# Performance work log

Measured on AMD Instinct MI355X. Metric: run time of the kernel, lower is better.

The kernel has to match this reference:

```python
import jax, jax.numpy as jnp
import numpy as np

IN_F, OUT_F = 512, 512
GRID_SIZE, SPLINE_ORDER = 5, 3
K = GRID_SIZE + SPLINE_ORDER  # 8 basis functions
B, S = 8, 1024


def setup_inputs() -> dict:
    key = jax.random.key(0)
    k1, k2, k3, k4, k5 = jax.random.split(key, 5)
    return {
        "x": jax.random.normal(k1, (B, S, IN_F), dtype=jnp.float32),
        "coeff": jax.random.normal(k2, (OUT_F, IN_F, K), dtype=jnp.float32),
        "scale_base": jax.random.normal(k3, (OUT_F, IN_F), dtype=jnp.float32) * 0.1,
        "scale_spline": jax.random.normal(k4, (OUT_F, IN_F), dtype=jnp.float32),
        "base_bias": jax.random.normal(k5, (OUT_F, IN_F), dtype=jnp.float32),
    }


def reference(x, coeff, scale_base, scale_spline, base_bias):
    batch = x.shape[0]
    in_f = x.shape[-1]
    k = coeff.shape[-1]

    xc = jnp.clip(x.reshape(-1, in_f), -1.0, 1.0)      # (N, in)
    base = jax.nn.silu(xc)                              # (N, in)

    # polynomial basis recurrence: b0 = 1, b1 = x, b_i = 2*x*b_{i-1} - 1
    bases = [jnp.ones_like(xc), xc]
    for _ in range(2, k):
        bases.append(2.0 * xc * bases[-1] - 1.0)
    basis = jnp.stack(bases[:k], axis=-1)               # (N, in, K)

    # spline[n,o] = sum_{i,k} scale_spline[o,i]*coeff[o,i,k]*basis[n,i,k]
    w_spline = scale_spline[..., None] * coeff          # (out, in, K)
    spline_term = jnp.einsum('nik,oik->no', basis, w_spline)
    base_term = base @ scale_base.T                     # (N, out)
    out = base_term + spline_term + jnp.sum(base_bias, axis=1)  # (N, out)

    out = out.reshape(batch, -1, base_bias.shape[0])    # (B, S, out)
    if out.shape[-2] == 1:
        out = out[..., 0, :]
    return out
```

## Files before the change

kernel.cpp:

```cpp
#include <hip/hip_runtime.h>
#include <hip/hip_bf16.h>

#define IN_FEAT 512
#define OUT_FEAT 512
#define NTOK 8192
#define KDIM 4096

#define BM 64
#define BN 128
#define BK 64

typedef short bf16x8 __attribute__((ext_vector_type(8)));
typedef float f32x4 __attribute__((ext_vector_type(4)));

static __device__ inline short f2bf(float f) {
    union { float f; unsigned u; } v; v.f = f;
    unsigned u = v.u;
    u += 0x7fffu + ((u >> 16) & 1u);
    return (short)(u >> 16);
}

static __device__ inline unsigned pack2bf(float f0, float f1) {
    union { float f; unsigned u; } a, b; a.f = f0; b.f = f1;
    return __builtin_amdgcn_perm(b.u + 0x8000u, a.u + 0x8000u, 0x07060302u);
}

static __device__ inline void gload_lds16(const short* g, short* l) {
    __builtin_amdgcn_global_load_lds(
        (const __attribute__((address_space(1))) unsigned int*)g,
        (__attribute__((address_space(3))) unsigned int*)l,
        16, 0, 0);
}

__global__ __launch_bounds__(256) void kan_prep(
    const float* __restrict__ coeff, const float* __restrict__ scale_base,
    const float* __restrict__ scale_spline, const float* __restrict__ base_bias,
    short* __restrict__ Wb, float* __restrict__ bias)
{
    int o = blockIdx.x;
    int tid = threadIdx.x;
    float local = 0.f;
#pragma unroll
    for (int rep = 0; rep < 2; ++rep) {
        int i = tid + rep * 256;
        size_t oi = (size_t)o * IN_FEAT + i;
        const float4* c4 = (const float4*)(coeff + oi * 8);
        float4 ca = c4[0], cb = c4[1];
        float ss = scale_spline[oi];
        float sb = scale_base[oi];
        local += base_bias[oi] + ss * ca.x;
        bf16x8 w;
        w[0] = f2bf(sb);
        w[1] = f2bf(ss * ca.y); w[2] = f2bf(ss * ca.z); w[3] = f2bf(ss * ca.w);
        w[4] = f2bf(ss * cb.x); w[5] = f2bf(ss * cb.y); w[6] = f2bf(ss * cb.z);
        w[7] = f2bf(ss * cb.w);
        *(bf16x8*)(Wb + (size_t)o * KDIM + (size_t)i * 8) = w;
    }
    __shared__ float red[4];
    for (int off = 32; off > 0; off >>= 1) local += __shfl_down(local, off, 64);
    int lane = tid & 63, wv = tid >> 6;
    if (lane == 0) red[wv] = local;
    __syncthreads();
    if (tid == 0) bias[o] = red[0] + red[1] + red[2] + red[3];
}

__global__ __launch_bounds__(256) void kan_gemm3(
    const float* __restrict__ x, const short* __restrict__ Wb,
    const float* __restrict__ bias, float* __restrict__ out)
{
    __shared__ __align__(16) short As[2][BM * BK];
    __shared__ __align__(16) short Bs[2][BN * BK];

    int tid = threadIdx.x;
    int nb = blockIdx.x & 3;
    int mb = blockIdx.x >> 2;
    int m0 = mb * BM, o0 = nb * BN;

    int lane = tid & 63, wv = tid >> 6;
    int wm = wv & 1, wn = wv >> 1;
    int qd = lane >> 4, ln15 = lane & 15;

    f32x4 acc[2][4];
#pragma unroll
    for (int a = 0; a < 2; ++a)
#pragma unroll
        for (int b = 0; b < 4; ++b) acc[a][b] = (f32x4)0.f;

    int tok = tid >> 2;
    int c0  = (tid & 3) * 2;
    const float2* xp = (const float2*)(x + (size_t)(m0 + tok) * IN_FEAT) + (tid & 3);

    int rg = lane >> 3;
    int c_log = (lane & 7) ^ rg;
    const short* Bg = Wb + (size_t)(o0 + wv * 32 + rg) * KDIM + c_log * 8;

#define GEN_CHUNK(xval, cc, buf)                                              \
    {                                                                         \
        float xc = fminf(fmaxf((xval), -1.f), 1.f);                           \
        float bse = xc / (1.f + __expf(-xc));                                 \
        float b2 = 2.f * xc * xc - 1.f;                                       \
        float b3 = 2.f * xc * b2 - 1.f;                                       \
        float b4 = 2.f * xc * b3 - 1.f;                                       \
        float b5 = 2.f * xc * b4 - 1.f;                                       \
        float b6 = 2.f * xc * b5 - 1.f;                                       \
        float b7 = 2.f * xc * b6 - 1.f;                                       \
        uint4 pk;                                                             \
        pk.x = pack2bf(bse, xc); pk.y = pack2bf(b2, b3);                      \
        pk.z = pack2bf(b4, b5);  pk.w = pack2bf(b6, b7);                      \
        *(uint4*)&As[buf][tok * BK + ((cc) ^ (tok & 7)) * 8] = pk;            \
    }

    {
        float2 xv = xp[0];
        GEN_CHUNK(xv.x, c0, 0);
        GEN_CHUNK(xv.y, c0 + 1, 0);
#pragma unroll
        for (int j = 0; j < 4; ++j)
            gload_lds16(Bg + (size_t)j * 8 * KDIM, &Bs[0][(wv * 32 + j * 8) * BK]);
    }

    int cur = 0;
    for (int it = 0; it < IN_FEAT / 8; ++it, cur ^= 1) {
        __syncthreads();
        if (it < IN_FEAT / 8 - 1) {
            int nxt = cur ^ 1;
#pragma unroll
            for (int j = 0; j < 4; ++j)
                gload_lds16(Bg + (it + 1) * BK + (size_t)j * 8 * KDIM,
                            &Bs[nxt][(wv * 32 + j * 8) * BK]);
            float2 xv = xp[(it + 1) * 4];
            GEN_CHUNK(xv.x, c0, nxt);
            GEN_CHUNK(xv.y, c0 + 1, nxt);
        }
#pragma unroll
        for (int kq = 0; kq < 2; ++kq) {
            bf16x8 af[2], bf[4];
#pragma unroll
            for (int fm = 0; fm < 2; ++fm) {
                int row = wm * 32 + fm * 16 + ln15;
                af[fm] = *(const bf16x8*)&As[cur][row * BK + ((kq * 4 + qd) ^ (row & 7)) * 8];
            }
#pragma unroll
            for (int fn = 0; fn < 4; ++fn) {
                int row = wn * 64 + fn * 16 + ln15;
                bf[fn] = *(const bf16x8*)&Bs[cur][row * BK + ((kq * 4 + qd) ^ (row & 7)) * 8];
            }
#pragma unroll
            for (int fm = 0; fm < 2; ++fm)
#pragma unroll
                for (int fn = 0; fn < 4; ++fn)
                    acc[fm][fn] = __builtin_amdgcn_mfma_f32_16x16x32_bf16(
                        af[fm], bf[fn], acc[fm][fn], 0, 0, 0);
        }
    }

#pragma unroll
    for (int fn = 0; fn < 4; ++fn) {
        int o = o0 + wn * 64 + fn * 16 + ln15;
        float bv = bias[o];
#pragma unroll
        for (int fm = 0; fm < 2; ++fm) {
            int r0 = m0 + wm * 32 + fm * 16 + qd * 4;
#pragma unroll
            for (int r = 0; r < 4; ++r)
                out[(size_t)(r0 + r) * OUT_FEAT + o] = acc[fm][fn][r] + bv;
        }
    }
#undef GEN_CHUNK
}

extern "C" void kernel_launch(void* const* d_in, const int* in_sizes, int n_in,
                              void* d_out, int out_size, void* d_ws, size_t ws_size,
                              hipStream_t stream) {
    const float* x            = (const float*)d_in[0];
    const float* coeff        = (const float*)d_in[1];
    const float* scale_base   = (const float*)d_in[2];
    const float* scale_spline = (const float*)d_in[3];
    const float* base_bias    = (const float*)d_in[4];
    float* out = (float*)d_out;

    short* Wb   = (short*)d_ws;
    float* bias = (float*)((char*)d_ws + (size_t)OUT_FEAT * KDIM * 2);

    kan_prep<<<OUT_FEAT, 256, 0, stream>>>(coeff, scale_base, scale_spline, base_bias, Wb, bias);
    kan_gemm3<<<(NTOK / BM) * (OUT_FEAT / BN), 256, 0, stream>>>(x, Wb, bias, out);
}
```

Baseline: 145.4 us.

## Reshape GEMM tile to 32x256 so each token's basis is generated once per half

Changes the block tile from 64 tokens x 128 outputs to 32 tokens x 256 outputs, with all four waves sharing the same A rows and each wave owning 64 output columns. Each thread now generates one basis chunk per iteration instead of two. This halves the redundant x loading and basis computation across output blocks, since only two column blocks now recompute the basis rather than four. In exchange each block streams twice as much weight data through LDS per iteration, so weight traffic per token rises, and the larger B tile increases LDS use. A launch-bounds hint for two blocks per CU is also added.

```diff
diff --git a/kernel.cpp b/kernel.cpp
--- a/kernel.cpp
+++ b/kernel.cpp
@@ -6,8 +6,8 @@
 #define NTOK 8192
 #define KDIM 4096
 
-#define BM 64
-#define BN 128
+#define BM 32
+#define BN 256
 #define BK 64
 
 typedef short bf16x8 __attribute__((ext_vector_type(8)));
@@ -64,7 +64,7 @@
     if (tid == 0) bias[o] = red[0] + red[1] + red[2] + red[3];
 }
 
-__global__ __launch_bounds__(256) void kan_gemm3(
+__global__ __launch_bounds__(256, 2) void kan_gemm4(
     const float* __restrict__ x, const short* __restrict__ Wb,
     const float* __restrict__ bias, float* __restrict__ out)
 {
@@ -72,12 +72,11 @@
     __shared__ __align__(16) short Bs[2][BN * BK];
 
     int tid = threadIdx.x;
-    int nb = blockIdx.x & 3;
-    int mb = blockIdx.x >> 2;
+    int nb = blockIdx.x & 1;
+    int mb = blockIdx.x >> 1;
     int m0 = mb * BM, o0 = nb * BN;
 
     int lane = tid & 63, wv = tid >> 6;
-    int wm = wv & 1, wn = wv >> 1;
     int qd = lane >> 4, ln15 = lane & 15;
 
     f32x4 acc[2][4];
@@ -86,15 +85,16 @@
 #pragma unroll
         for (int b = 0; b < 4; ++b) acc[a][b] = (f32x4)0.f;
 
-    int tok = tid >> 2;
-    int c0  = (tid & 3) * 2;
-    const float2* xp = (const float2*)(x + (size_t)(m0 + tok) * IN_FEAT) + (tid & 3);
+    int tok = tid >> 3;
+    int inp = tid & 7;
+    const float* xq = x + (size_t)(m0 + tok) * IN_FEAT + inp;
+    int aoff = tok * BK + (inp ^ (tok & 7)) * 8;
 
     int rg = lane >> 3;
     int c_log = (lane & 7) ^ rg;
-    const short* Bg = Wb + (size_t)(o0 + wv * 32 + rg) * KDIM + c_log * 8;
+    const short* Bg = Wb + (size_t)(o0 + wv * 64 + rg) * KDIM + c_log * 8;
 
-#define GEN_CHUNK(xval, cc, buf)                                              \
+#define GEN_CHUNK(xval, buf)                                                  \
     {                                                                         \
         float xc = fminf(fmaxf((xval), -1.f), 1.f);                           \
         float bse = xc / (1.f + __expf(-xc));                                 \
@@ -107,16 +107,15 @@
         uint4 pk;                                                             \
         pk.x = pack2bf(bse, xc); pk.y = pack2bf(b2, b3);                      \
         pk.z = pack2bf(b4, b5);  pk.w = pack2bf(b6, b7);                      \
-        *(uint4*)&As[buf][tok * BK + ((cc) ^ (tok & 7)) * 8] = pk;            \
+        *(uint4*)&As[buf][aoff] = pk;                                         \
     }
 
     {
-        float2 xv = xp[0];
-        GEN_CHUNK(xv.x, c0, 0);
-        GEN_CHUNK(xv.y, c0 + 1, 0);
 #pragma unroll
-        for (int j = 0; j < 4; ++j)
-            gload_lds16(Bg + (size_t)j * 8 * KDIM, &Bs[0][(wv * 32 + j * 8) * BK]);
+        for (int j = 0; j < 8; ++j)
+            gload_lds16(Bg + (size_t)j * 8 * KDIM, &Bs[0][(wv * 64 + j * 8) * BK]);
+        float xv = xq[0];
+        GEN_CHUNK(xv, 0);
     }
 
     int cur = 0;
@@ -124,49 +123,48 @@
         __syncthreads();
         if (it < IN_FEAT / 8 - 1) {
             int nxt = cur ^ 1;
+            const short* bsrc = Bg + (it + 1) * BK;
 #pragma unroll
-            for (int j = 0; j < 4; ++j)
-                gload_lds16(Bg + (it + 1) * BK + (size_t)j * 8 * KDIM,
-                            &Bs[nxt][(wv * 32 + j * 8) * BK]);
-            float2 xv = xp[(it + 1) * 4];
-            GEN_CHUNK(xv.x, c0, nxt);
-            GEN_CHUNK(xv.y, c0 + 1, nxt);
+            for (int j = 0; j < 8; ++j)
+                gload_lds16(bsrc + (size_t)j * 8 * KDIM, &Bs[nxt][(wv * 64 + j * 8) * BK]);
+            float xv = xq[(it + 1) * 8];
+            GEN_CHUNK(xv, nxt);
         }
 #pragma unroll
         for (int kq = 0; kq < 2; ++kq) {
-            bf16x8 af[2], bf[4];
+            bf16x8 af[2], bfv[4];
 #pragma unroll
             for (int fm = 0; fm < 2; ++fm) {
-                int row = wm * 32 + fm * 16 + ln15;
+                int row = fm * 16 + ln15;
                 af[fm] = *(const bf16x8*)&As[cur][row * BK + ((kq * 4 + qd) ^ (row & 7)) * 8];
             }
 #pragma unroll
             for (int fn = 0; fn < 4; ++fn) {
-                int row = wn * 64 + fn * 16 + ln15;
-                bf[fn] = *(const bf16x8*)&Bs[cur][row * BK + ((kq * 4 + qd) ^ (row & 7)) * 8];
+                int row = wv * 64 + fn * 16 + ln15;
+                bfv[fn] = *(const bf16x8*)&Bs[cur][row * BK + ((kq * 4 + qd) ^ (row & 7)) * 8];
             }
 #pragma unroll
             for (int fm = 0; fm < 2; ++fm)
 #pragma unroll
                 for (int fn = 0; fn < 4; ++fn)
                     acc[fm][fn] = __builtin_amdgcn_mfma_f32_16x16x32_bf16(
-                        af[fm], bf[fn], acc[fm][fn], 0, 0, 0);
+                        af[fm], bfv[fn], acc[fm][fn], 0, 0, 0);
         }
     }
+#undef GEN_CHUNK
 
 #pragma unroll
     for (int fn = 0; fn < 4; ++fn) {
-        int o = o0 + wn * 64 + fn * 16 + ln15;
+        int o = o0 + wv * 64 + fn * 16 + ln15;
         float bv = bias[o];
 #pragma unroll
         for (int fm = 0; fm < 2; ++fm) {
-            int r0 = m0 + wm * 32 + fm * 16 + qd * 4;
+            int r0 = m0 + fm * 16 + qd * 4;
 #pragma unroll
             for (int r = 0; r < 4; ++r)
                 out[(size_t)(r0 + r) * OUT_FEAT + o] = acc[fm][fn][r] + bv;
         }
     }
-#undef GEN_CHUNK
 }
 
 extern "C" void kernel_launch(void* const* d_in, const int* in_sizes, int n_in,
@@ -183,5 +181,5 @@
     float* bias = (float*)((char*)d_ws + (size_t)OUT_FEAT * KDIM * 2);
 
     kan_prep<<<OUT_FEAT, 256, 0, stream>>>(coeff, scale_base, scale_spline, base_bias, Wb, bias);
-    kan_gemm3<<<(NTOK / BM) * (OUT_FEAT / BN), 256, 0, stream>>>(x, Wb, bias, out);
+    kan_gemm4<<<(NTOK / BM) * (OUT_FEAT / BN), 256, 0, stream>>>(x, Wb, bias, out);
 }
```

Measured after the change: 154.3 us. 6.1% more time.

## Generate spline basis in registers from raw x slab instead of LDS bf16 tile

Applied to the files above, without the earlier changes.

The A operand is no longer expanded into a bf16 basis tile in shared memory. Raw fp32 x values go into a small padded transposed slab, and each wave builds its MFMA A fragments directly in registers just before the multiply. This cuts LDS footprint and A-tile traffic and adds a launch-bounds occupancy hint, which could let more blocks fit per CU. The cost is redundant basis and SiLU work, since each wave with a different wn recomputes the same fragments, and a fast reciprocal replaces the division.

```diff
diff --git a/kernel.cpp b/kernel.cpp
--- a/kernel.cpp
+++ b/kernel.cpp
@@ -9,6 +9,7 @@
 #define BM 64
 #define BN 128
 #define BK 64
+#define XPAD 72
 
 typedef short bf16x8 __attribute__((ext_vector_type(8)));
 typedef float f32x4 __attribute__((ext_vector_type(4)));
@@ -23,6 +24,24 @@
 static __device__ inline unsigned pack2bf(float f0, float f1) {
     union { float f; unsigned u; } a, b; a.f = f0; b.f = f1;
     return __builtin_amdgcn_perm(b.u + 0x8000u, a.u + 0x8000u, 0x07060302u);
+}
+
+static __device__ inline bf16x8 gen_chunk(float xv) {
+    float xc = fminf(fmaxf(xv, -1.f), 1.f);
+    float e  = __expf(-xc);
+    float bse = xc * __builtin_amdgcn_rcpf(1.f + e);
+    float b2 = 2.f * xc * xc - 1.f;
+    float b3 = 2.f * xc * b2 - 1.f;
+    float b4 = 2.f * xc * b3 - 1.f;
+    float b5 = 2.f * xc * b4 - 1.f;
+    float b6 = 2.f * xc * b5 - 1.f;
+    float b7 = 2.f * xc * b6 - 1.f;
+    union { uint4 u; bf16x8 v; } r;
+    r.u.x = pack2bf(bse, xc);
+    r.u.y = pack2bf(b2, b3);
+    r.u.z = pack2bf(b4, b5);
+    r.u.w = pack2bf(b6, b7);
+    return r.v;
 }
 
 static __device__ inline void gload_lds16(const short* g, short* l) {
@@ -64,12 +83,12 @@
     if (tid == 0) bias[o] = red[0] + red[1] + red[2] + red[3];
 }
 
-__global__ __launch_bounds__(256) void kan_gemm3(
+__global__ __launch_bounds__(256, 4) void kan_gemm8(
     const float* __restrict__ x, const short* __restrict__ Wb,
     const float* __restrict__ bias, float* __restrict__ out)
 {
-    __shared__ __align__(16) short As[2][BM * BK];
     __shared__ __align__(16) short Bs[2][BN * BK];
+    __shared__ __align__(16) float xslab[2][8 * XPAD];
 
     int tid = threadIdx.x;
     int nb = blockIdx.x & 3;
@@ -86,37 +105,21 @@
 #pragma unroll
         for (int b = 0; b < 4; ++b) acc[a][b] = (f32x4)0.f;
 
-    int tok = tid >> 2;
-    int c0  = (tid & 3) * 2;
-    const float2* xp = (const float2*)(x + (size_t)(m0 + tok) * IN_FEAT) + (tid & 3);
-
     int rg = lane >> 3;
     int c_log = (lane & 7) ^ rg;
     const short* Bg = Wb + (size_t)(o0 + wv * 32 + rg) * KDIM + c_log * 8;
 
-#define GEN_CHUNK(xval, cc, buf)                                              \
-    {                                                                         \
-        float xc = fminf(fmaxf((xval), -1.f), 1.f);                           \
-        float bse = xc / (1.f + __expf(-xc));                                 \
-        float b2 = 2.f * xc * xc - 1.f;                                       \
-        float b3 = 2.f * xc * b2 - 1.f;                                       \
-        float b4 = 2.f * xc * b3 - 1.f;                                       \
-        float b5 = 2.f * xc * b4 - 1.f;                                       \
-        float b6 = 2.f * xc * b5 - 1.f;                                       \
-        float b7 = 2.f * xc * b6 - 1.f;                                       \
-        uint4 pk;                                                             \
-        pk.x = pack2bf(bse, xc); pk.y = pack2bf(b2, b3);                      \
-        pk.z = pack2bf(b4, b5);  pk.w = pack2bf(b6, b7);                      \
-        *(uint4*)&As[buf][tok * BK + ((cc) ^ (tok & 7)) * 8] = pk;            \
-    }
+    int xrow = tid >> 2, xc0 = (tid & 3) * 2;
+    const float* xg = x + (size_t)(m0 + xrow) * IN_FEAT + xc0;
+    int so0 = xc0 * XPAD + xrow, so1 = (xc0 + 1) * XPAD + xrow;
 
     {
-        float2 xv = xp[0];
-        GEN_CHUNK(xv.x, c0, 0);
-        GEN_CHUNK(xv.y, c0 + 1, 0);
 #pragma unroll
         for (int j = 0; j < 4; ++j)
             gload_lds16(Bg + (size_t)j * 8 * KDIM, &Bs[0][(wv * 32 + j * 8) * BK]);
+        float2 xv = *(const float2*)xg;
+        xslab[0][so0] = xv.x;
+        xslab[0][so1] = xv.y;
     }
 
     int cur = 0;
@@ -124,33 +127,34 @@
         __syncthreads();
         if (it < IN_FEAT / 8 - 1) {
             int nxt = cur ^ 1;
+            const short* bsrc = Bg + (it + 1) * BK;
 #pragma unroll
             for (int j = 0; j < 4; ++j)
-                gload_lds16(Bg + (it + 1) * BK + (size_t)j * 8 * KDIM,
-                            &Bs[nxt][(wv * 32 + j * 8) * BK]);
-            float2 xv = xp[(it + 1) * 4];
-            GEN_CHUNK(xv.x, c0, nxt);
-            GEN_CHUNK(xv.y, c0 + 1, nxt);
+                gload_lds16(bsrc + (size_t)j * 8 * KDIM, &Bs[nxt][(wv * 32 + j * 8) * BK]);
+            float2 xv = *(const float2*)(xg + (it + 1) * 8);
+            xslab[nxt][so0] = xv.x;
+            xslab[nxt][so1] = xv.y;
         }
 #pragma unroll
         for (int kq = 0; kq < 2; ++kq) {
-            bf16x8 af[2], bf[4];
+            int inp = kq * 4 + qd;
+            bf16x8 af[2], bfv[4];
 #pragma unroll
-            for (int fm = 0; fm < 2; ++fm) {
-                int row = wm * 32 + fm * 16 + ln15;
-                af[fm] = *(const bf16x8*)&As[cur][row * BK + ((kq * 4 + qd) ^ (row & 7)) * 8];
+            for (int f = 0; f < 2; ++f) {
+                float xv_ = xslab[cur][inp * XPAD + wm * 32 + f * 16 + ln15];
+                af[f] = gen_chunk(xv_);
             }
 #pragma unroll
             for (int fn = 0; fn < 4; ++fn) {
                 int row = wn * 64 + fn * 16 + ln15;
-                bf[fn] = *(const bf16x8*)&Bs[cur][row * BK + ((kq * 4 + qd) ^ (row & 7)) * 8];
+                bfv[fn] = *(const bf16x8*)&Bs[cur][row * BK + ((kq * 4 + qd) ^ (row & 7)) * 8];
             }
 #pragma unroll
-            for (int fm = 0; fm < 2; ++fm)
+            for (int f = 0; f < 2; ++f)
 #pragma unroll
                 for (int fn = 0; fn < 4; ++fn)
-                    acc[fm][fn] = __builtin_amdgcn_mfma_f32_16x16x32_bf16(
-                        af[fm], bf[fn], acc[fm][fn], 0, 0, 0);
+                    acc[f][fn] = __builtin_amdgcn_mfma_f32_16x16x32_bf16(
+                        af[f], bfv[fn], acc[f][fn], 0, 0, 0);
         }
     }
 
@@ -159,14 +163,13 @@
         int o = o0 + wn * 64 + fn * 16 + ln15;
         float bv = bias[o];
 #pragma unroll
-        for (int fm = 0; fm < 2; ++fm) {
-            int r0 = m0 + wm * 32 + fm * 16 + qd * 4;
+        for (int f = 0; f < 2; ++f) {
+            int r0 = m0 + wm * 32 + f * 16 + qd * 4;
 #pragma unroll
             for (int r = 0; r < 4; ++r)
-                out[(size_t)(r0 + r) * OUT_FEAT + o] = acc[fm][fn][r] + bv;
+                out[(size_t)(r0 + r) * OUT_FEAT + o] = acc[f][fn][r] + bv;
         }
     }
-#undef GEN_CHUNK
 }
 
 extern "C" void kernel_launch(void* const* d_in, const int* in_sizes, int n_in,
@@ -183,5 +186,5 @@
     float* bias = (float*)((char*)d_ws + (size_t)OUT_FEAT * KDIM * 2);
 
     kan_prep<<<OUT_FEAT, 256, 0, stream>>>(coeff, scale_base, scale_spline, base_bias, Wb, bias);
-    kan_gemm3<<<(NTOK / BM) * (OUT_FEAT / BN), 256, 0, stream>>>(x, Wb, bias, out);
+    kan_gemm8<<<(NTOK / BM) * (OUT_FEAT / BN), 256, 0, stream>>>(x, Wb, bias, out);
 }
```

New measurement: 139.2 us. -4.2%, faster.
